# Kernel tuning notes

Measured on AMD Instinct MI355X. Metric: run time of the kernel, lower is better.

The kernel has to match this reference:

```python
import jax, jax.numpy as jnp
import numpy as np
from jax import lax

NUM_HEADS = 4
SIDE = 5  # side_dwconv


def setup_inputs() -> dict:
    key = jax.random.key(0)
    ks = jax.random.split(key, 7)
    B, C, H, W = 2, 128, 56, 56
    return {
        "x": jax.random.normal(ks[0], (B, C, H, W), dtype=jnp.float32),
        "qkv_w": jax.random.normal(ks[1], (3 * C, C), dtype=jnp.float32) * 0.02,
        "qkv_b": jax.random.normal(ks[2], (3 * C,), dtype=jnp.float32) * 0.02,
        "lepe_w": jax.random.normal(ks[3], (C, 1, SIDE, SIDE), dtype=jnp.float32) * 0.02,
        "lepe_b": jax.random.normal(ks[4], (C,), dtype=jnp.float32) * 0.02,
        "proj_w": jax.random.normal(ks[5], (C, C), dtype=jnp.float32) * 0.02,
        "proj_b": jax.random.normal(ks[6], (C,), dtype=jnp.float32) * 0.02,
    }


def reference(x, qkv_w, qkv_b, lepe_w, lepe_b, proj_w, proj_b):
    B, C, H, W = x.shape
    nh = NUM_HEADS
    hd = C // nh
    scale = hd ** (-0.5)
    N = H * W

    # 1x1 conv qkv == channel matmul
    qkv = jnp.einsum('oc,bchw->bohw', qkv_w, x) + qkv_b[None, :, None, None]
    q, k, v = jnp.split(qkv, 3, axis=1)  # each [B, C, H, W]

    qr = q.reshape(B, nh, hd, N)
    kr = k.reshape(B, nh, hd, N)
    vr = v.reshape(B, nh, hd, N)

    # attn = q^T k over head_dim -> [B, nh, N, N]
    attn = jnp.einsum('bhdn,bhdm->bhnm', qr, kr) * scale
    attn = jax.nn.softmax(attn, axis=-1)

    # out = attn @ v^T, then permute back to [B, C, H, W]
    out = jnp.einsum('bhnm,bhdm->bhdn', attn, vr).reshape(B, C, H, W)

    # depthwise LePE conv on v, fused with residual add
    pad = SIDE // 2
    lepe = lax.conv_general_dilated(
        v, lepe_w, window_strides=(1, 1), padding=[(pad, pad), (pad, pad)],
        dimension_numbers=('NCHW', 'OIHW', 'NCHW'), feature_group_count=C,
    ) + lepe_b[None, :, None, None]
    out = out + lepe

    # 1x1 conv proj
    out = jnp.einsum('oc,bchw->bohw', proj_w, out) + proj_b[None, :, None, None]
    return out
```

## Files before the change

kernel.cpp:

```cpp
#include <hip/hip_runtime.h>

typedef __bf16 bf16x8 __attribute__((ext_vector_type(8)));
typedef __bf16 bf16x4 __attribute__((ext_vector_type(4)));
typedef float  f32x4  __attribute__((ext_vector_type(4)));

#define NPIX  3136
#define WIMG  56
#define CCH   128
#define NH    4
#define HD    32
#define NSPLIT 8
#define QSCALE 0.2550565470841439f

#if __has_builtin(__builtin_amdgcn_exp2f)
#define FEXP2(x) __builtin_amdgcn_exp2f(x)
#else
#define FEXP2(x) __expf((x) * 0.6931471805599453f)
#endif


__device__ __forceinline__ int perm_inv(int k) {
    return (((k >> 5) & 1) * 2 + ((k >> 2) & 1)) * 16 + (((k >> 3) & 3) * 4) + (k & 3);
}

__global__ __launch_bounds__(256) void k_qkv(
    const float* __restrict__ x, const float* __restrict__ qkv_w,
    const float* __restrict__ qkv_b,
    __bf16* __restrict__ qT, __bf16* __restrict__ kT,
    __bf16* __restrict__ vT, __bf16* __restrict__ vP)
{
    __shared__ __bf16 xl[32][136];
    const int tid = threadIdx.x;
    const int w = tid >> 6, lane = tid & 63;
    const int col = lane & 15, g = lane >> 4;
    const int px0 = blockIdx.x * 32;
    const int slab = blockIdx.y;
    const int b = blockIdx.z;
    const int obase = slab * 128 + w * 32;
    const int kbase = px0 & ~63;
    const int khalf = px0 & 32;

    {
        const int px = tid & 31, cq = tid >> 5;
        const float* xp = x + (size_t)b * CCH * NPIX + px0 + px;
        #pragma unroll
        for (int i = 0; i < 4; ++i) {
            const int c0 = cq * 4 + i * 32;
            const float v0 = xp[(size_t)(c0 + 0) * NPIX];
            const float v1 = xp[(size_t)(c0 + 1) * NPIX];
            const float v2 = xp[(size_t)(c0 + 2) * NPIX];
            const float v3 = xp[(size_t)(c0 + 3) * NPIX];
            bf16x4 bv = {(__bf16)v0, (__bf16)v1, (__bf16)v2, (__bf16)v3};
            *(bf16x4*)&xl[px][c0] = bv;
        }
    }
    __syncthreads();

    f32x4 acc[2][2];
    #pragma unroll
    for (int ot = 0; ot < 2; ++ot)
        #pragma unroll
        for (int a = 0; a < 2; ++a) acc[ot][a] = (f32x4){0.f, 0.f, 0.f, 0.f};

    #pragma unroll
    for (int ks = 0; ks < 4; ++ks) {
        const int c0 = ks * 32 + g * 8;
        #pragma unroll
        for (int ot = 0; ot < 2; ++ot) {
            const float* wrow = qkv_w + (size_t)(obase + ot * 16 + col) * CCH + c0;
            const float4 wA = *(const float4*)(wrow);
            const float4 wB = *(const float4*)(wrow + 4);
            bf16x8 af = {(__bf16)wA.x, (__bf16)wA.y, (__bf16)wA.z, (__bf16)wA.w,
                         (__bf16)wB.x, (__bf16)wB.y, (__bf16)wB.z, (__bf16)wB.w};
            #pragma unroll
            for (int a = 0; a < 2; ++a) {
                const bf16x8 bf_ = *(const bf16x8*)&xl[16 * a + col][c0];
                acc[ot][a] = __builtin_amdgcn_mfma_f32_16x16x32_bf16(af, bf_, acc[ot][a], 0, 0, 0);
            }
        }
    }

    #pragma unroll
    for (int ot = 0; ot < 2; ++ot) {
        const int orow = obase + ot * 16 + g * 4;
        const f32x4 bias4 = *(const f32x4*)(qkv_b + orow);
        if (slab == 0) {
            const int o = orow, h = o >> 5, d0 = o & 31;
            __bf16* dst = qT + ((size_t)(b * NH + h) * NPIX) * HD + d0;
            #pragma unroll
            for (int a = 0; a < 2; ++a) {
                const int px = px0 + 16 * a + col;
                bf16x4 v;
                #pragma unroll
                for (int r = 0; r < 4; ++r) v[r] = (__bf16)((acc[ot][a][r] + bias4[r]) * QSCALE);
                *(bf16x4*)(dst + (size_t)px * HD) = v;
            }
        } else if (slab == 1) {
            const int o = orow - 128, h = o >> 5, d0 = o & 31;
            __bf16* dst = kT + ((size_t)(b * NH + h) * NPIX) * HD + d0;
            #pragma unroll
            for (int a = 0; a < 2; ++a) {
                const int s = perm_inv(khalf + 16 * a + col);
                bf16x4 v;
                #pragma unroll
                for (int r = 0; r < 4; ++r) v[r] = (__bf16)(acc[ot][a][r] + bias4[r]);
                *(bf16x4*)(dst + (size_t)(kbase + s) * HD) = v;
            }
        } else {
            const int c = orow - 256;
            #pragma unroll
            for (int a = 0; a < 2; ++a) {
                const int px = px0 + 16 * a + col;
                const int s = perm_inv(khalf + 16 * a + col);
                bf16x4 v;
                #pragma unroll
                for (int r = 0; r < 4; ++r) v[r] = (__bf16)(acc[ot][a][r] + bias4[r]);
                *(bf16x4*)(vT + ((size_t)(b * NPIX + px)) * CCH + c) = v;
                #pragma unroll
                for (int r = 0; r < 4; ++r)
                    vP[((size_t)(b * CCH + c + r)) * NPIX + kbase + s] = v[r];
            }
        }
    }
}

__global__ __launch_bounds__(256, 4) void k_attn(
    const __bf16* __restrict__ qT, const __bf16* __restrict__ kT,
    const __bf16* __restrict__ vP,
    __bf16* __restrict__ pO, float* __restrict__ pl)
{
    __shared__ __bf16 Kl[2][64][32];
    __shared__ __bf16 Vl[2][32][72];

    const int tid = threadIdx.x;
    const int w = tid >> 6, lane = tid & 63;
    const int col = lane & 15, g = lane >> 4;
    const int qt = blockIdx.x * 4 + w;
    const bool valid = qt < 49;
    const int qtc = valid ? qt : 48;
    const int bh = blockIdx.y, sp = blockIdx.z;
    const int b = bh >> 2, h = bh & 3;
    const int qbase = qtc * 64;
    const size_t headoff = (size_t)bh * NPIX * HD;
    const int c0h = h * HD;

    const __bf16* qbp = qT + headoff + (size_t)(qbase + col) * HD + g * 8;
    const bf16x8 aq0 = *(const bf16x8*)(qbp);
    const bf16x8 aq1 = *(const bf16x8*)(qbp + 16 * HD);
    const bf16x8 aq2 = *(const bf16x8*)(qbp + 32 * HD);
    const bf16x8 aq3 = *(const bf16x8*)(qbp + 48 * HD);

    const __bf16 one = (__bf16)1.0f;
    const bf16x8 ones = {one, one, one, one, one, one, one, one};

    f32x4 O00 = {0,0,0,0}, O01 = {0,0,0,0}, O10 = {0,0,0,0}, O11 = {0,0,0,0};
    f32x4 O20 = {0,0,0,0}, O21 = {0,0,0,0}, O30 = {0,0,0,0}, O31 = {0,0,0,0};
    f32x4 La0 = {0,0,0,0}, La1 = {0,0,0,0}, La2 = {0,0,0,0}, La3 = {0,0,0,0};

    const __bf16* kTh = kT + headoff;
    const int vr = tid >> 3;
    const int vo = (tid & 7) * 8;
    const __bf16* vsrc = vP + (size_t)(b * CCH + c0h + vr) * NPIX + vo;

    const int cs = (49 * sp) >> 3, ce = (49 * (sp + 1)) >> 3;

#define STAGE(BUF, CHUNK) do { const int _k0 = (CHUNK) * 64;                           \
        *(bf16x8*)(&Kl[BUF][0][0] + tid * 8) =                                         \
            *(const bf16x8*)(kTh + (size_t)_k0 * HD + tid * 8);                        \
        *(bf16x8*)(&Vl[BUF][vr][vo]) = *(const bf16x8*)(vsrc + _k0);                   \
    } while (0)

#define SQH(AQ, O0R, O1R, LAR)  do {                                                   \
        f32x4 s0 = __builtin_amdgcn_mfma_f32_16x16x32_bf16(ck0, AQ, zz, 0, 0, 0);      \
        f32x4 s1 = __builtin_amdgcn_mfma_f32_16x16x32_bf16(ck1, AQ, zz, 0, 0, 0);      \
        bf16x8 P0 = {(__bf16)FEXP2(s0[0]), (__bf16)FEXP2(s0[1]),                       \
                     (__bf16)FEXP2(s0[2]), (__bf16)FEXP2(s0[3]),                       \
                     (__bf16)FEXP2(s1[0]), (__bf16)FEXP2(s1[1]),                       \
                     (__bf16)FEXP2(s1[2]), (__bf16)FEXP2(s1[3])};                      \
        O0R = __builtin_amdgcn_mfma_f32_16x16x32_bf16(vv00, P0, O0R, 0, 0, 0);         \
        O1R = __builtin_amdgcn_mfma_f32_16x16x32_bf16(vv10, P0, O1R, 0, 0, 0);         \
        LAR = __builtin_amdgcn_mfma_f32_16x16x32_bf16(ones, P0, LAR, 0, 0, 0);         \
        f32x4 s2 = __builtin_amdgcn_mfma_f32_16x16x32_bf16(ck2, AQ, zz, 0, 0, 0);      \
        f32x4 s3 = __builtin_amdgcn_mfma_f32_16x16x32_bf16(ck3, AQ, zz, 0, 0, 0);      \
        bf16x8 P1 = {(__bf16)FEXP2(s2[0]), (__bf16)FEXP2(s2[1]),                       \
                     (__bf16)FEXP2(s2[2]), (__bf16)FEXP2(s2[3]),                       \
                     (__bf16)FEXP2(s3[0]), (__bf16)FEXP2(s3[1]),                       \
                     (__bf16)FEXP2(s3[2]), (__bf16)FEXP2(s3[3])};                      \
        O0R = __builtin_amdgcn_mfma_f32_16x16x32_bf16(vv01, P1, O0R, 0, 0, 0);         \
        O1R = __builtin_amdgcn_mfma_f32_16x16x32_bf16(vv11, P1, O1R, 0, 0, 0);         \
        LAR = __builtin_amdgcn_mfma_f32_16x16x32_bf16(ones, P1, LAR, 0, 0, 0);         \
    } while (0)

#define COMPUTE(CUR) do {                                                              \
        const __bf16* Kb = &Kl[CUR][0][0];                                             \
        const __bf16* Vb = &Vl[CUR][0][0];                                             \
        const bf16x8 ck0 = *(const bf16x8*)(Kb + (      col) * 32 + g * 8);            \
        const bf16x8 ck1 = *(const bf16x8*)(Kb + (16 + col) * 32 + g * 8);             \
        const bf16x8 ck2 = *(const bf16x8*)(Kb + (32 + col) * 32 + g * 8);             \
        const bf16x8 ck3 = *(const bf16x8*)(Kb + (48 + col) * 32 + g * 8);             \
        const bf16x8 vv00 = *(const bf16x8*)(Vb + (      col) * 72      + g * 8);      \
        const bf16x8 vv01 = *(const bf16x8*)(Vb + (      col) * 72 + 32 + g * 8);      \
        const bf16x8 vv10 = *(const bf16x8*)(Vb + (16 + col) * 72      + g * 8);       \
        const bf16x8 vv11 = *(const bf16x8*)(Vb + (16 + col) * 72 + 32 + g * 8);       \
        const f32x4 zz = {0.f, 0.f, 0.f, 0.f};                                         \
        SQH(aq0, O00, O01, La0);                                                       \
        SQH(aq1, O10, O11, La1);                                                       \
        SQH(aq2, O20, O21, La2);                                                       \
        SQH(aq3, O30, O31, La3);                                                       \
    } while (0)

    STAGE(0, cs);
    __syncthreads();
    for (int cc = cs; cc < ce; ++cc) {
        const int cur = (cc - cs) & 1;
        if (cc + 1 < ce) STAGE(cur ^ 1, cc + 1);
        COMPUTE(cur);
        __syncthreads();
    }
#undef STAGE
#undef SQH
#undef COMPUTE

    if (!valid) return;
    const int t = bh * 49 + qt;
    __bf16* po = pO + ((size_t)t * NSPLIT + sp) * 64 * 32;
    float* plp = pl + ((size_t)t * NSPLIT + sp) * 64;
#define STQH(QH, O0R, O1R, LAR) do {                                                   \
        bf16x4 v0 = {(__bf16)O0R[0], (__bf16)O0R[1], (__bf16)O0R[2], (__bf16)O0R[3]};  \
        bf16x4 v1 = {(__bf16)O1R[0], (__bf16)O1R[1], (__bf16)O1R[2], (__bf16)O1R[3]};  \
        *(bf16x4*)(po + ((QH) * 16 + col) * 32      + g * 4) = v0;                     \
        *(bf16x4*)(po + ((QH) * 16 + col) * 32 + 16 + g * 4) = v1;                     \
        if (g == 0) plp[(QH) * 16 + col] = LAR[0];                                     \
    } while (0)
    STQH(0, O00, O01, La0);
    STQH(1, O10, O11, La1);
    STQH(2, O20, O21, La2);
    STQH(3, O30, O31, La3);
#undef STQH
}

__global__ __launch_bounds__(256) void k_reduce(
    const __bf16* __restrict__ pO, const float* __restrict__ pl,
    const __bf16* __restrict__ vT,
    const float* __restrict__ lepe_w, const float* __restrict__ lepe_b,
    __bf16* __restrict__ attnT)
{
    __shared__ float wl[32][25];
    __shared__ float bl[32];
    const int tid = threadIdx.x;
    const int qt = blockIdx.x, bh = blockIdx.y;
    const int b = bh >> 2, h = bh & 3;
    const int c0h = h * HD;

    for (int i = tid; i < 800; i += 256) ((float*)wl)[i] = lepe_w[c0h * 25 + i];
    if (tid < 32) bl[tid] = lepe_b[c0h + tid];
    __syncthreads();

    const int q  = tid >> 2;
    const int dg = (tid & 3) * 8;
    const size_t t = (size_t)bh * 49 + qt;

    float lt = 0.f;
    float o[8] = {0.f, 0.f, 0.f, 0.f, 0.f, 0.f, 0.f, 0.f};
    #pragma unroll
    for (int s = 0; s < NSPLIT; ++s) {
        lt += pl[(t * NSPLIT + s) * 64 + q];
        const bf16x8 pv = *(const bf16x8*)(pO + ((t * NSPLIT + s) * 64 + q) * 32 + dg);
        #pragma unroll
        for (int i = 0; i < 8; ++i) o[i] += (float)pv[i];
    }
    const float linv = 1.0f / lt;
    #pragma unroll
    for (int i = 0; i < 8; ++i) o[i] = o[i] * linv + bl[dg + i];

    const int px = qt * 64 + q;
    const int py = px / WIMG, pxx = px % WIMG;
    const __bf16* vtb = vT + ((size_t)b * NPIX) * CCH + c0h + dg;
    #pragma unroll
    for (int dy = 0; dy < 5; ++dy) {
        const int yy = py + dy - 2;
        if (yy < 0 || yy >= WIMG) continue;
        #pragma unroll
        for (int dx = 0; dx < 5; ++dx) {
            const int xx = pxx + dx - 2;
            if (xx < 0 || xx >= WIMG) continue;
            const bf16x8 vv = *(const bf16x8*)(vtb + (size_t)(yy * WIMG + xx) * CCH);
            const int tap = dy * 5 + dx;
            #pragma unroll
            for (int i = 0; i < 8; ++i) o[i] += (float)vv[i] * wl[dg + i][tap];
        }
    }
    bf16x8 ov = {(__bf16)o[0], (__bf16)o[1], (__bf16)o[2], (__bf16)o[3],
                 (__bf16)o[4], (__bf16)o[5], (__bf16)o[6], (__bf16)o[7]};
    *(bf16x8*)(attnT + ((size_t)(b * NPIX + px)) * CCH + c0h + dg) = ov;
}

__global__ __launch_bounds__(256) void k_proj(
    const __bf16* __restrict__ attnT, const float* __restrict__ proj_w,
    const float* __restrict__ proj_b, float* __restrict__ out)
{
    const int tid = threadIdx.x;
    const int w = tid >> 6, lane = tid & 63;
    const int col = lane & 15, g = lane >> 4;
    const int px0 = blockIdx.x * 32 + (w >> 1) * 16;
    const int obase = blockIdx.y * 32 + (w & 1) * 16;
    const int b = blockIdx.z;

    const float* wrow = proj_w + (size_t)(obase + col) * CCH;
    const __bf16* abase = attnT + (size_t)(b * NPIX + px0) * CCH;

    f32x4 acc = {0.f, 0.f, 0.f, 0.f};
    #pragma unroll
    for (int ks = 0; ks < 4; ++ks) {
        const int c0 = ks * 32 + g * 8;
        const float4 wA = *(const float4*)(wrow + c0);
        const float4 wB = *(const float4*)(wrow + c0 + 4);
        bf16x8 af = {(__bf16)wA.x, (__bf16)wA.y, (__bf16)wA.z, (__bf16)wA.w,
                     (__bf16)wB.x, (__bf16)wB.y, (__bf16)wB.z, (__bf16)wB.w};
        const bf16x8 bf_ = *(const bf16x8*)(abase + (size_t)col * CCH + c0);
        acc = __builtin_amdgcn_mfma_f32_16x16x32_bf16(af, bf_, acc, 0, 0, 0);
    }

    const f32x4 pb = *(const f32x4*)(proj_b + obase + g * 4);
    #pragma unroll
    for (int r = 0; r < 4; ++r)
        out[(size_t)(b * CCH + obase + g * 4 + r) * NPIX + px0 + col] = acc[r] + pb[r];
}

extern "C" void kernel_launch(void* const* d_in, const int* in_sizes, int n_in,
                              void* d_out, int out_size, void* d_ws, size_t ws_size,
                              hipStream_t stream)
{
    const float* x      = (const float*)d_in[0];
    const float* qkv_w  = (const float*)d_in[1];
    const float* qkv_b  = (const float*)d_in[2];
    const float* lepe_w = (const float*)d_in[3];
    const float* lepe_b = (const float*)d_in[4];
    const float* proj_w = (const float*)d_in[5];
    const float* proj_b = (const float*)d_in[6];
    float* out = (float*)d_out;

    char* p = (char*)d_ws;
    __bf16* qT    = (__bf16*)p;  p += (size_t)2 * NH * NPIX * HD * 2;
    __bf16* kT    = (__bf16*)p;  p += (size_t)2 * NH * NPIX * HD * 2;
    __bf16* vT    = (__bf16*)p;  p += (size_t)2 * NPIX * CCH * 2;
    __bf16* vP    = (__bf16*)p;  p += (size_t)2 * CCH * NPIX * 2;
    __bf16* attnT = (__bf16*)p;  p += (size_t)2 * NPIX * CCH * 2;
    __bf16* pO    = (__bf16*)p;  p += (size_t)392 * NSPLIT * 64 * 32 * 2;
    float*  pl    = (float*)p;

    k_qkv   <<<dim3(98, 3, 2), dim3(256), 0, stream>>>(x, qkv_w, qkv_b, qT, kT, vT, vP);
    k_attn  <<<dim3(13, 8, 8), dim3(256), 0, stream>>>(qT, kT, vP, pO, pl);
    k_reduce<<<dim3(49, 8),    dim3(256), 0, stream>>>(pO, pl, vT, lepe_w, lepe_b, attnT);
    k_proj  <<<dim3(98, 4, 2), dim3(256), 0, stream>>>(attnT, proj_w, proj_b, out);
}
```

Before: 119.8 us.

## Fuse split-KV reduce, LePE conv and output projection into one kernel

Merges the split-reduction/LePE kernel and the projection kernel into a single kernel. Each block handles 16 pixels across all 128 channels, keeps the combined attention+LePE tile in LDS, and runs the projection MFMAs directly from LDS. This removes one launch and the bf16 attnT round trip through global memory. In exchange every block reloads the full LePE weight table (128x25) into LDS, and the grid changes shape to 392 blocks.

```diff
diff --git a/kernel.cpp b/kernel.cpp
--- a/kernel.cpp
+++ b/kernel.cpp
@@ -239,92 +239,95 @@
 #undef STQH
 }
 
-__global__ __launch_bounds__(256) void k_reduce(
+__global__ __launch_bounds__(256) void k_rproj(
     const __bf16* __restrict__ pO, const float* __restrict__ pl,
     const __bf16* __restrict__ vT,
     const float* __restrict__ lepe_w, const float* __restrict__ lepe_b,
-    __bf16* __restrict__ attnT)
+    const float* __restrict__ proj_w, const float* __restrict__ proj_b,
+    float* __restrict__ out)
 {
-    __shared__ float wl[32][25];
-    __shared__ float bl[32];
+    __shared__ __bf16 at[16][136];
+    __shared__ float  wl[CCH][25];
+    __shared__ float  bl[CCH];
     const int tid = threadIdx.x;
-    const int qt = blockIdx.x, bh = blockIdx.y;
-    const int b = bh >> 2, h = bh & 3;
-    const int c0h = h * HD;
-
-    for (int i = tid; i < 800; i += 256) ((float*)wl)[i] = lepe_w[c0h * 25 + i];
-    if (tid < 32) bl[tid] = lepe_b[c0h + tid];
+    const int pb = blockIdx.x;
+    const int b  = blockIdx.y;
+    const int qt = pb >> 2;
+    const int qs = (pb & 3) * 16;
+    const int px0 = qt * 64 + qs;
+
+    for (int i = tid; i < CCH * 25; i += 256) ((float*)wl)[i] = lepe_w[i];
+    if (tid < CCH) bl[tid] = lepe_b[tid];
     __syncthreads();
 
-    const int q  = tid >> 2;
-    const int dg = (tid & 3) * 8;
-    const size_t t = (size_t)bh * 49 + qt;
-
-    float lt = 0.f;
-    float o[8] = {0.f, 0.f, 0.f, 0.f, 0.f, 0.f, 0.f, 0.f};
-    #pragma unroll
-    for (int s = 0; s < NSPLIT; ++s) {
-        lt += pl[(t * NSPLIT + s) * 64 + q];
-        const bf16x8 pv = *(const bf16x8*)(pO + ((t * NSPLIT + s) * 64 + q) * 32 + dg);
-        #pragma unroll
-        for (int i = 0; i < 8; ++i) o[i] += (float)pv[i];
-    }
-    const float linv = 1.0f / lt;
-    #pragma unroll
-    for (int i = 0; i < 8; ++i) o[i] = o[i] * linv + bl[dg + i];
-
-    const int px = qt * 64 + q;
-    const int py = px / WIMG, pxx = px % WIMG;
-    const __bf16* vtb = vT + ((size_t)b * NPIX) * CCH + c0h + dg;
-    #pragma unroll
-    for (int dy = 0; dy < 5; ++dy) {
-        const int yy = py + dy - 2;
-        if (yy < 0 || yy >= WIMG) continue;
-        #pragma unroll
-        for (int dx = 0; dx < 5; ++dx) {
-            const int xx = pxx + dx - 2;
-            if (xx < 0 || xx >= WIMG) continue;
-            const bf16x8 vv = *(const bf16x8*)(vtb + (size_t)(yy * WIMG + xx) * CCH);
-            const int tap = dy * 5 + dx;
-            #pragma unroll
-            for (int i = 0; i < 8; ++i) o[i] += (float)vv[i] * wl[dg + i][tap];
-        }
-    }
-    bf16x8 ov = {(__bf16)o[0], (__bf16)o[1], (__bf16)o[2], (__bf16)o[3],
-                 (__bf16)o[4], (__bf16)o[5], (__bf16)o[6], (__bf16)o[7]};
-    *(bf16x8*)(attnT + ((size_t)(b * NPIX + px)) * CCH + c0h + dg) = ov;
-}
-
-__global__ __launch_bounds__(256) void k_proj(
-    const __bf16* __restrict__ attnT, const float* __restrict__ proj_w,
-    const float* __restrict__ proj_b, float* __restrict__ out)
-{
-    const int tid = threadIdx.x;
+    {
+        const int px = tid >> 4;
+        const int cg = (tid & 15) * 8;
+        const int h  = cg >> 5;
+        const int dg = cg & 31;
+        const int q  = qs + px;
+        const size_t t = (size_t)(b * NH + h) * 49 + qt;
+
+        float lt = 0.f;
+        float o[8] = {0.f, 0.f, 0.f, 0.f, 0.f, 0.f, 0.f, 0.f};
+        #pragma unroll
+        for (int s = 0; s < NSPLIT; ++s) {
+            lt += pl[(t * NSPLIT + s) * 64 + q];
+            const bf16x8 pv = *(const bf16x8*)(pO + ((t * NSPLIT + s) * 64 + q) * 32 + dg);
+            #pragma unroll
+            for (int i = 0; i < 8; ++i) o[i] += (float)pv[i];
+        }
+        const float linv = 1.0f / lt;
+        #pragma unroll
+        for (int i = 0; i < 8; ++i) o[i] = o[i] * linv + bl[cg + i];
+
+        const int P = px0 + px;
+        const int py = P / WIMG, pxx = P % WIMG;
+        const __bf16* vtb = vT + ((size_t)b * NPIX) * CCH + cg;
+        #pragma unroll
+        for (int dy = 0; dy < 5; ++dy) {
+            const int yy = py + dy - 2;
+            if (yy < 0 || yy >= WIMG) continue;
+            #pragma unroll
+            for (int dx = 0; dx < 5; ++dx) {
+                const int xx = pxx + dx - 2;
+                if (xx < 0 || xx >= WIMG) continue;
+                const bf16x8 vv = *(const bf16x8*)(vtb + (size_t)(yy * WIMG + xx) * CCH);
+                const int tap = dy * 5 + dx;
+                #pragma unroll
+                for (int i = 0; i < 8; ++i) o[i] += (float)vv[i] * wl[cg + i][tap];
+            }
+        }
+        bf16x8 ov = {(__bf16)o[0], (__bf16)o[1], (__bf16)o[2], (__bf16)o[3],
+                     (__bf16)o[4], (__bf16)o[5], (__bf16)o[6], (__bf16)o[7]};
+        *(bf16x8*)&at[px][cg] = ov;
+    }
+    __syncthreads();
+
     const int w = tid >> 6, lane = tid & 63;
     const int col = lane & 15, g = lane >> 4;
-    const int px0 = blockIdx.x * 32 + (w >> 1) * 16;
-    const int obase = blockIdx.y * 32 + (w & 1) * 16;
-    const int b = blockIdx.z;
-
-    const float* wrow = proj_w + (size_t)(obase + col) * CCH;
-    const __bf16* abase = attnT + (size_t)(b * NPIX + px0) * CCH;
-
-    f32x4 acc = {0.f, 0.f, 0.f, 0.f};
+    const int obase = w * 32;
+
     #pragma unroll
-    for (int ks = 0; ks < 4; ++ks) {
-        const int c0 = ks * 32 + g * 8;
-        const float4 wA = *(const float4*)(wrow + c0);
-        const float4 wB = *(const float4*)(wrow + c0 + 4);
-        bf16x8 af = {(__bf16)wA.x, (__bf16)wA.y, (__bf16)wA.z, (__bf16)wA.w,
-                     (__bf16)wB.x, (__bf16)wB.y, (__bf16)wB.z, (__bf16)wB.w};
-        const bf16x8 bf_ = *(const bf16x8*)(abase + (size_t)col * CCH + c0);
-        acc = __builtin_amdgcn_mfma_f32_16x16x32_bf16(af, bf_, acc, 0, 0, 0);
-    }
-
-    const f32x4 pb = *(const f32x4*)(proj_b + obase + g * 4);
-    #pragma unroll
-    for (int r = 0; r < 4; ++r)
-        out[(size_t)(b * CCH + obase + g * 4 + r) * NPIX + px0 + col] = acc[r] + pb[r];
+    for (int ot = 0; ot < 2; ++ot) {
+        const float* wrow = proj_w + (size_t)(obase + ot * 16 + col) * CCH;
+        f32x4 acc = {0.f, 0.f, 0.f, 0.f};
+        #pragma unroll
+        for (int ks = 0; ks < 4; ++ks) {
+            const int c0 = ks * 32 + g * 8;
+            const float4 wA = *(const float4*)(wrow + c0);
+            const float4 wB = *(const float4*)(wrow + c0 + 4);
+            bf16x8 af = {(__bf16)wA.x, (__bf16)wA.y, (__bf16)wA.z, (__bf16)wA.w,
+                         (__bf16)wB.x, (__bf16)wB.y, (__bf16)wB.z, (__bf16)wB.w};
+            const bf16x8 bf_ = *(const bf16x8*)&at[col][c0];
+            acc = __builtin_amdgcn_mfma_f32_16x16x32_bf16(af, bf_, acc, 0, 0, 0);
+        }
+        const f32x4 pb4 = *(const f32x4*)(proj_b + obase + ot * 16 + g * 4);
+        #pragma unroll
+        for (int r = 0; r < 4; ++r)
+            out[(size_t)(b * CCH + obase + ot * 16 + g * 4 + r) * NPIX + px0 + col] =
+                acc[r] + pb4[r];
+    }
 }
 
 extern "C" void kernel_launch(void* const* d_in, const int* in_sizes, int n_in,
@@ -341,16 +344,15 @@
     float* out = (float*)d_out;
 
     char* p = (char*)d_ws;
-    __bf16* qT    = (__bf16*)p;  p += (size_t)2 * NH * NPIX * HD * 2;
-    __bf16* kT    = (__bf16*)p;  p += (size_t)2 * NH * NPIX * HD * 2;
-    __bf16* vT    = (__bf16*)p;  p += (size_t)2 * NPIX * CCH * 2;
-    __bf16* vP    = (__bf16*)p;  p += (size_t)2 * CCH * NPIX * 2;
-    __bf16* attnT = (__bf16*)p;  p += (size_t)2 * NPIX * CCH * 2;
-    __bf16* pO    = (__bf16*)p;  p += (size_t)392 * NSPLIT * 64 * 32 * 2;
-    float*  pl    = (float*)p;
-
-    k_qkv   <<<dim3(98, 3, 2), dim3(256), 0, stream>>>(x, qkv_w, qkv_b, qT, kT, vT, vP);
-    k_attn  <<<dim3(13, 8, 8), dim3(256), 0, stream>>>(qT, kT, vP, pO, pl);
-    k_reduce<<<dim3(49, 8),    dim3(256), 0, stream>>>(pO, pl, vT, lepe_w, lepe_b, attnT);
-    k_proj  <<<dim3(98, 4, 2), dim3(256), 0, stream>>>(attnT, proj_w, proj_b, out);
-}
+    __bf16* qT = (__bf16*)p;  p += (size_t)2 * NH * NPIX * HD * 2;
+    __bf16* kT = (__bf16*)p;  p += (size_t)2 * NH * NPIX * HD * 2;
+    __bf16* vT = (__bf16*)p;  p += (size_t)2 * NPIX * CCH * 2;
+    __bf16* vP = (__bf16*)p;  p += (size_t)2 * CCH * NPIX * 2;
+    __bf16* pO = (__bf16*)p;  p += (size_t)392 * NSPLIT * 64 * 32 * 2;
+    float*  pl = (float*)p;
+
+    k_qkv  <<<dim3(98, 3, 2), dim3(256), 0, stream>>>(x, qkv_w, qkv_b, qT, kT, vT, vP);
+    k_attn <<<dim3(13, 8, 8), dim3(256), 0, stream>>>(qT, kT, vP, pO, pl);
+    k_rproj<<<dim3(196, 2),   dim3(256), 0, stream>>>(pO, pl, vT, lepe_w, lepe_b,
+                                                      proj_w, proj_b, out);
+}
```

Measured after the change: 117.5 us (median of 2 runs). About the same (-1.9%).
